# Optimization experiments

Hardware: AMD Instinct MI355X
Metric: run time of the kernel (lower is better)

Reference implementation:

```python
import jax, jax.numpy as jnp
import numpy as np

B, S, IN_DIM, LATENT, SYM = 16, 256, 512, 512, 128
NUM_NODES, NUM_CODES, MAX_OPS, MAX_BUS = 4, 512, 4, 32
HALT_EPS, MAX_SEQ = 1e-3, 256


def setup_inputs() -> dict:
    key = jax.random.key(0)
    ks = jax.random.split(key, 10)

    def lin(k, out_d, in_d, pre=()):
        kw, kb = jax.random.split(k)
        lim = 1.0 / np.sqrt(in_d).astype(np.float32)
        w = jax.random.uniform(kw, pre + (out_d, in_d), minval=-lim, maxval=lim, dtype=jnp.float32)
        b = jax.random.uniform(kb, pre + (out_d,), minval=-lim, maxval=lim, dtype=jnp.float32)
        return w, b

    x = jax.random.normal(ks[0], (B, S, IN_DIM), jnp.float32)
    ipw, ipb = lin(ks[1], LATENT, IN_DIM)
    tp = jax.random.normal(ks[2], (1, MAX_SEQ, LATENT), jnp.float32)
    N = (NUM_NODES,)
    sw, sb = lin(ks[3], SYM, LATENT, N)
    qw, qb = lin(ks[4], 1, SYM, N)
    rw, rb = lin(ks[5], LATENT, 2 * LATENT, N)
    c1w, c1b = lin(ks[6], LATENT, LATENT + SYM, N)
    c2w, c2b = lin(ks[7], LATENT, LATENT, N)
    cb = jax.random.normal(ks[8], (NUM_NODES, NUM_CODES, SYM), jnp.float32)
    return {"x": x, "input_proj_w": ipw, "input_proj_b": ipb, "token_prompts": tp,
            "sym_w": sw, "sym_b": sb, "qry_w": qw, "qry_b": qb,
            "read_w": rw, "read_b": rb, "c1_w": c1w, "c1_b": c1b,
            "c2_w": c2w, "c2_b": c2b, "codebook": cb}


def _forward(x, input_proj_w, input_proj_b, token_prompts, sym_w, sym_b, qry_w, qry_b,
             read_w, read_b, c1_w, c1_b, c2_w, c2_b, codebook):
    Bx, Sx, _ = x.shape
    N = Bx * Sx
    # input projection + positional prompts
    out = jnp.einsum('bsi,li->bsl', x, input_proj_w) + input_proj_b + token_prompts[:, :Sx, :]
    prev_out = out
    active = jnp.ones((Bx, Sx), bool)
    token_tags = jnp.zeros((Bx, Sx, SYM), x.dtype)
    # TensorBus rolling buffers ([max_bus, B, S, dim]); with default cfg the roll branch never fires
    sym_buf = jnp.zeros((MAX_BUS, Bx, Sx, SYM), x.dtype)          # slot 0 = zero tags (initial append)
    out_buf = jnp.zeros((MAX_BUS, Bx, Sx, LATENT), x.dtype).at[0].set(out)
    msg_mask = jnp.zeros((MAX_BUS,), bool).at[0].set(True)
    ptr = 1  # static python int: appends are a fixed unrolled schedule (1 + MAX_OPS*NUM_NODES <= MAX_BUS)
    slot_ids = jnp.arange(MAX_BUS)

    for t in range(MAX_OPS):
        # snapshot of active messages for this op step (get_active)
        snap_active = msg_mask & (slot_ids < ptr)                  # [MAX_BUS]
        syms_flat = sym_buf.reshape(MAX_BUS, N, SYM)
        outs_flat = out_buf.reshape(MAX_BUS, N, LATENT)
        keep_all = jnp.ones((MAX_BUS,), bool)
        for n in range(NUM_NODES):
            # relevance of each bus message per token; inactive slots masked out of argmax
            rel = jnp.einsum('tnd,d->tn', syms_flat, qry_w[n, 0]) + qry_b[n, 0]
            rel = jnp.where(snap_active[:, None], rel, jnp.asarray(-1e9, rel.dtype))
            top = jnp.argmax(rel, axis=0)                          # [N] chosen message per token
            chosen = jnp.take_along_axis(outs_flat, top[None, :, None], axis=0)[0]  # [N, LATENT]
            bus_ctx = chosen.reshape(Bx, Sx, LATENT)
            z = jnp.concatenate([out, bus_ctx], axis=-1)
            z_read = jnp.einsum('bsk,lk->bsl', z, read_w[n]) + read_b[n]
            raw_sym = jnp.einsum('bsl,dl->bsd', z_read, sym_w[n]) + sym_b[n]
            # EMA quantizer (eval): nearest codebook entry by euclidean distance
            flat = raw_sym.reshape(-1, SYM)
            cbn = codebook[n]
            d2 = (jnp.sum(flat * flat, axis=-1, keepdims=True)
                  - 2.0 * flat @ cbn.T + jnp.sum(cbn * cbn, axis=-1))
            idx = jnp.argmin(d2, axis=-1)
            quant = cbn[idx].reshape(Bx, Sx, SYM)
            h = jnp.concatenate([z_read, quant], axis=-1)
            hid = jax.nn.relu(jnp.einsum('bsk,lk->bsl', h, c1_w[n]) + c1_b[n])
            node_out = jnp.einsum('bsl,ol->bso', hid, c2_w[n]) + c2_b[n] + out
            # halting / selective update
            delta = jnp.linalg.norm(node_out - prev_out, axis=-1)
            halt = (delta < HALT_EPS) & active
            assigned = active if t > 0 else jnp.ones_like(active)
            upd = assigned & jnp.logical_not(halt)
            out = jnp.where(upd[..., None], node_out, out)
            token_tags = jnp.where(upd[..., None], quant, token_tags)
            # bus.append
            sym_buf = sym_buf.at[ptr].set(quant)
            out_buf = out_buf.at[ptr].set(node_out)
            msg_mask = msg_mask.at[ptr].set(True)
            ptr += 1
            # keep_mask: messages never selected by any token stay alive
            counts = jnp.zeros((MAX_BUS,), jnp.int32).at[top].add(1)
            keep_all = keep_all & (counts == 0)
            active = active & jnp.logical_not(halt)
            prev_out = out
        # mark_consumed: ones over valid slots ANDed with per-node keep masks at snapshot-active
        # slots (inactive/new slots get True -> faithful to the torch init_global_mask quirk)
        msg_mask = (slot_ids < ptr) & keep_all
    return out


def reference(x, input_proj_w, input_proj_b, token_prompts, sym_w, sym_b, qry_w, qry_b,
              read_w, read_b, c1_w, c1_b, c2_w, c2_b, codebook):
    return _forward(x, input_proj_w, input_proj_b, token_prompts, sym_w, sym_b, qry_w, qry_b,
                    read_w, read_b, c1_w, c1_b, c2_w, c2_b, codebook)
```

## Files before the change

kernel.cpp:

```cpp
#include <hip/hip_runtime.h>
#include <math.h>

namespace {

typedef _Float16 f16;
typedef __attribute__((ext_vector_type(8))) _Float16 f16x8;
typedef __attribute__((ext_vector_type(4))) float f32x4;

constexpr int TOK = 4096;
constexpr int DL  = 512;
constexpr int DS  = 128;
constexpr int NC  = 512;
constexpr int NSLOT = 13;

__device__ __forceinline__ float wsum(float v){
  #pragma unroll
  for(int o=32;o>0;o>>=1) v += __shfl_xor(v,o);
  return v;
}

__device__ __forceinline__ void gload16(const void* g, void* l){
  __builtin_amdgcn_global_load_lds(
      (const __attribute__((address_space(1))) unsigned int*)g,
      (__attribute__((address_space(3))) unsigned int*)l, 16, 0, 0);
}

__device__ __forceinline__ int slotb(int row, int g){
  return (((row ^ ((row>>2)&1))<<2) | (g ^ (row&3))) << 4;
}

template<int AMODE,int EPI>
__global__ __launch_bounds__(256,2) void mgemm(
    const f16* __restrict__ A1h, const f16* __restrict__ A1l,
    const f16* __restrict__ A2h, const f16* __restrict__ A2l,
    const f16* __restrict__ Bh, const f16* __restrict__ Bl,
    const float* __restrict__ bias, const float* __restrict__ res,
    float* __restrict__ Cf, f16* __restrict__ Ch, f16* __restrict__ Cl,
    f16* __restrict__ C2h, f16* __restrict__ C2l,
    float* __restrict__ scpv, int* __restrict__ scpi, int* __restrict__ idxg,
    const float* __restrict__ relc, const int* __restrict__ msg,
    int* __restrict__ cons, int pt, int node,
    int K, int K0)
{
  constexpr int SMB = 16384;
  __shared__ __align__(16) char smem[3*SMB];
  __shared__ int gsel[64];
  __shared__ float redv[4][32];
  __shared__ int   redi[4][32];
  const int tid = threadIdx.x, w = tid>>6, l = tid&63;
  const int m0 = blockIdx.x*64, n0 = blockIdx.y*64;
  const int NK = K>>5, SW = K0>>5;

  if(AMODE==1){
    if(tid<64){
      int m = m0+tid;
      float best = -1e9f; int bs = 0;
      for(int s=0;s<pt;s++){
        float v = msg[s] ? relc[(size_t)((s<<2)+node)*TOK + m] : -1e9f;
        if(v > best){ best=v; bs=s; }
      }
      gsel[tid]=bs;
      cons[bs]=1;
    }
    __syncthreads();
  }
  if(AMODE==2){
    if(tid<64){
      int m = m0+tid;
      float bv = -INFINITY; int bi = 0;
      #pragma unroll
      for(int y=0;y<8;y++){
        float v = scpv[(size_t)y*TOK + m];
        if(v > bv){ bv=v; bi=scpi[(size_t)y*TOK + m]; }
      }
      gsel[tid]=bi;
      idxg[m]=bi;
    }
    __syncthreads();
  }

  const f16* sp[4]; const f16* sp2[4]; int loff[4];
  #pragma unroll
  for(int i=0;i<4;i++){
    int c = 4*w+i;
    int isA = (c<8);
    int plane = isA ? (c>>2) : ((c-8)>>2);
    int cidx  = isA ? (c&3)  : ((c-8)&3);
    loff[i] = (isA?0:8192) + plane*4096 + cidx*1024;
    int s = (cidx<<6) + l;
    int rp = s>>2, row = rp ^ ((rp>>2)&1), g = (s&3) ^ (row&3);
    int g8 = g<<3;
    if(isA){
      int m = m0 + row;
      const f16* p1 = (plane? A1l : A1h) + ((size_t)m<<9) + g8;
      sp[i] = p1;
      if(AMODE==1)      sp2[i] = (plane? A2l : A2h) + ((size_t)gsel[row]<<21) + ((size_t)m<<9) + g8;
      else if(AMODE==2) sp2[i] = (plane? A2l : A2h) + ((size_t)gsel[row]<<7) + g8;
      else              sp2[i] = p1;
    } else {
      sp[i] = (plane? Bl : Bh) + (size_t)(n0+row)*K + g8;
      sp2[i] = sp[i];
    }
  }

  const int wr = w>>1, wc = w&1, q = l>>4, r = l&15;
  int aoff[2], boff[2];
  #pragma unroll
  for(int i=0;i<2;i++) aoff[i] = slotb(32*wr + 16*i + r, q);
  #pragma unroll
  for(int j=0;j<2;j++) boff[j] = 8192 + slotb(32*wc + 16*j + r, q);

  f32x4 acc1[2][2] = {}, acc2[2][2] = {};

  auto advance = [&](int snext){
    #pragma unroll
    for(int i=0;i<4;i++){
      if(AMODE!=0 && (4*w+i)<8 && snext==SW) sp[i] = sp2[i];
      else                                    sp[i] += 32;
    }
  };

  #pragma unroll
  for(int i=0;i<4;i++) gload16(sp[i], smem + loff[i]);
  advance(1);
  #pragma unroll
  for(int i=0;i<4;i++) gload16(sp[i], smem + SMB + loff[i]);
  advance(2);
  asm volatile("s_waitcnt vmcnt(4)" ::: "memory");
  __builtin_amdgcn_s_barrier();

  int roff = 0, soff = 2*SMB;
  for(int kt=0; kt<NK; ++kt){
    const char* Lb = smem + roff;
    f16x8 ah[2], al[2], bh[2], bl[2];
    #pragma unroll
    for(int i=0;i<2;i++){
      ah[i] = *(const f16x8*)(Lb + aoff[i]);
      al[i] = *(const f16x8*)(Lb + 4096 + aoff[i]);
    }
    #pragma unroll
    for(int j=0;j<2;j++){
      bh[j] = *(const f16x8*)(Lb + boff[j]);
      bl[j] = *(const f16x8*)(Lb + 4096 + boff[j]);
    }
    if(kt+2 < NK){
      #pragma unroll
      for(int i=0;i<4;i++) gload16(sp[i], smem + soff + loff[i]);
      advance(kt+3);
    }
    #pragma unroll
    for(int i=0;i<2;i++)
      #pragma unroll
      for(int j=0;j<2;j++){
        acc1[i][j] = __builtin_amdgcn_mfma_f32_16x16x32_f16(ah[i], bh[j], acc1[i][j], 0,0,0);
        acc2[i][j] = __builtin_amdgcn_mfma_f32_16x16x32_f16(ah[i], bl[j], acc2[i][j], 0,0,0);
        acc2[i][j] = __builtin_amdgcn_mfma_f32_16x16x32_f16(al[i], bh[j], acc2[i][j], 0,0,0);
      }
    if(kt+2 < NK){
      asm volatile("s_waitcnt vmcnt(4)" ::: "memory");
      __builtin_amdgcn_s_barrier();
    } else if(kt+1 < NK){
      asm volatile("s_waitcnt vmcnt(0)" ::: "memory");
      __builtin_amdgcn_s_barrier();
    }
    roff = (roff==2*SMB)? 0 : roff+SMB;
    soff = (soff==2*SMB)? 0 : soff+SMB;
  }

  if(EPI!=1){
    #pragma unroll
    for(int i=0;i<2;i++)
      #pragma unroll
      for(int j=0;j<2;j++)
        #pragma unroll
        for(int rr=0;rr<4;rr++){
          int rowm = m0 + 32*wr + 16*i + 4*q + rr;
          int coln = n0 + 32*wc + 16*j + r;
          size_t o = ((size_t)rowm<<9) + coln;
          float v = acc1[i][j][rr] + acc2[i][j][rr]*(1.0f/2048.0f) + bias[coln];
          if(EPI==2) v = fmaxf(v, 0.f);
          if(EPI==3) v += res[o];
          if(EPI==4) v += res[(((size_t)(rowm&255))<<9) + coln];
          if(EPI==3 || EPI==4) Cf[o] = v;
          if(EPI==0 || EPI==2 || EPI==4){
            f16 h = (f16)v;
            Ch[o] = h; Cl[o] = (f16)((v-(float)h)*2048.0f);
          }
          if((EPI==3 || EPI==4) && C2h){
            f16 h = (f16)v;
            C2h[o] = h; C2l[o] = (f16)((v-(float)h)*2048.0f);
          }
        }
  } else {
    #pragma unroll
    for(int i=0;i<2;i++)
      #pragma unroll
      for(int rr=0;rr<4;rr++){
        float v0 = acc1[i][0][rr] + acc2[i][0][rr]*(1.0f/2048.0f) + bias[n0+32*wc+r];
        float v1 = acc1[i][1][rr] + acc2[i][1][rr]*(1.0f/2048.0f) + bias[n0+32*wc+16+r];
        float bv; int bc;
        if(v1 > v0){ bv=v1; bc=n0+32*wc+16+r; } else { bv=v0; bc=n0+32*wc+r; }
        #pragma unroll
        for(int o=1;o<16;o<<=1){
          float ov = __shfl_xor(bv,o); int oi = __shfl_xor(bc,o);
          if(ov>bv || (ov==bv && oi<bc)){ bv=ov; bc=oi; }
        }
        if(r==0){ redv[w][16*i+4*q+rr]=bv; redi[w][16*i+4*q+rr]=bc; }
      }
    __syncthreads();
    if(tid<64){
      int wr2 = tid>>5, li = tid&31;
      float bv = redv[2*wr2][li]; int bc = redi[2*wr2][li];
      float ov = redv[2*wr2+1][li]; int oi = redi[2*wr2+1][li];
      if(ov>bv || (ov==bv && oi<bc)){ bv=ov; bc=oi; }
      scpv[(size_t)blockIdx.y*TOK + m0 + tid] = bv;
      scpi[(size_t)blockIdx.y*TOK + m0 + tid] = bc;
    }
  }
}

__global__ void split_k(const float* __restrict__ src, f16* __restrict__ hi,
                        f16* __restrict__ lo, int n){
  for(int i = blockIdx.x*256 + threadIdx.x; i < n; i += gridDim.x*256){
    float v = src[i];
    f16 h = (f16)v;
    hi[i] = h;
    lo[i] = (f16)((v - (float)h)*2048.0f);
  }
}

struct SplitArg { const float* src; f16* hi; f16* lo; int n; };
struct SplitArgs5 { SplitArg a[5]; };
__global__ void splitm_k(SplitArgs5 A){
  int stride = gridDim.x*256;
  #pragma unroll
  for(int s=0;s<5;s++){
    const float* src = A.a[s].src; f16* hi = A.a[s].hi; f16* lo = A.a[s].lo;
    int n = A.a[s].n;
    for(int i = blockIdx.x*256 + threadIdx.x; i < n; i += stride){
      float v = src[i];
      f16 h = (f16)v;
      hi[i] = h;
      lo[i] = (f16)((v - (float)h)*2048.0f);
    }
  }
}

__global__ __launch_bounds__(256)
void wcomb_k(const float* __restrict__ A, const float* __restrict__ Wall,
             float* __restrict__ C)
{
  constexpr int T=256;
  __shared__ float As[32][68];
  __shared__ float Ws[32][132];
  const int tid = threadIdx.x;
  const int m0 = blockIdx.x*64, n0 = blockIdx.y*128;
  const float* W = Wall + (size_t)(m0>>9)*DS*DL;
  const int ty = tid>>4, tx = tid&15;
  float4 pa[2], pw[4];
  auto loadA = [&](int k0){
    #pragma unroll
    for(int it=0; it<2; ++it){
      int v = tid + T*it; int rr = v>>3, c4 = v&7;
      pa[it] = *(const float4*)(A + (size_t)(m0+rr)*DS + k0 + (c4<<2));
    }
  };
  auto loadW = [&](int k0){
    #pragma unroll
    for(int it=0; it<4; ++it){
      int v = tid + T*it; int rr = v>>5, c4 = v&31;
      pw[it] = *(const float4*)(W + (size_t)(k0+rr)*DL + n0 + (c4<<2));
    }
  };
  float acc[4][8];
  #pragma unroll
  for(int i=0;i<4;i++)
    #pragma unroll
    for(int j=0;j<8;j++) acc[i][j]=0.f;
  loadA(0); loadW(0);
  for(int k0=0; k0<DS; k0+=32){
    __syncthreads();
    #pragma unroll
    for(int it=0; it<2; ++it){
      int v = tid + T*it; int rr=v>>3, c4=v&7;
      As[(c4<<2)+0][rr]=pa[it].x; As[(c4<<2)+1][rr]=pa[it].y;
      As[(c4<<2)+2][rr]=pa[it].z; As[(c4<<2)+3][rr]=pa[it].w;
    }
    #pragma unroll
    for(int it=0; it<4; ++it){
      int v = tid + T*it; int rr=v>>5, c4=v&31;
      *(float4*)&Ws[rr][c4<<2] = pw[it];
    }
    __syncthreads();
    if(k0+32 < DS){ loadA(k0+32); loadW(k0+32); }
    #pragma unroll
    for(int kk=0; kk<32; kk++){
      float4 a4 = *(const float4*)&As[kk][ty<<2];
      float4 b0 = *(const float4*)&Ws[kk][tx<<2];
      float4 b1 = *(const float4*)&Ws[kk][64+(tx<<2)];
      float a[4]={a4.x,a4.y,a4.z,a4.w};
      float b[8]={b0.x,b0.y,b0.z,b0.w,b1.x,b1.y,b1.z,b1.w};
      #pragma unroll
      for(int i=0;i<4;i++)
        #pragma unroll
        for(int j=0;j<8;j++) acc[i][j] = fmaf(a[i], b[j], acc[i][j]);
    }
  }
  #pragma unroll
  for(int i=0;i<4;i++){
    int m = m0 + (ty<<2) + i;
    #pragma unroll
    for(int j=0;j<8;j++){
      int n = n0 + ((j<4)? (tx<<2)+j : 64+(tx<<2)+(j-4));
      C[((size_t)m<<9)+n] = acc[i][j];
    }
  }
}

__global__ void init_k(int* __restrict__ msg, int* __restrict__ act,
                       float* __restrict__ relc, const float* __restrict__ qb,
                       int* __restrict__ cons){
  int i = blockIdx.x*256 + threadIdx.x;
  if(i < TOK){
    act[i] = 1;
    #pragma unroll
    for(int nn=0;nn<4;nn++) relc[nn*TOK + i] = qb[nn];
  }
  if(i < 32){ msg[i] = (i==0) ? 1 : 0; cons[i] = 0; }
}

__global__ void bias2_k(const float* __restrict__ cb, const float* __restrict__ sb,
                        float* __restrict__ b2){
  int row = blockIdx.x*4 + (threadIdx.x>>6);
  int lane = threadIdx.x&63;
  const float* cv = cb + ((size_t)row<<7);
  const float* sbn = sb + ((row>>9)<<7);
  float c0=cv[lane], c1=cv[lane+64];
  float nrm = c0*c0 + c1*c1;
  float dt  = c0*sbn[lane] + c1*sbn[lane+64];
  nrm = wsum(nrm); dt = wsum(dt);
  if(lane==0) b2[row] = dt - 0.5f*nrm;
}

__global__ void mupdate_k(const float* __restrict__ no_, float* __restrict__ out,
                          f16* __restrict__ outh, f16* __restrict__ outl,
                          float* __restrict__ relc, const int* __restrict__ idx,
                          const float* __restrict__ cbn, const float* __restrict__ qw,
                          const float* __restrict__ qb, int* __restrict__ act,
                          int* __restrict__ cons, int* __restrict__ msg,
                          int t, int ptr, int pe){
  int m = blockIdx.x*4 + (threadIdx.x>>6);
  int lane = threadIdx.x&63;
  const float* nrow = no_ + ((size_t)m<<9);
  float* orow = out + ((size_t)m<<9);
  float nv[8]; float s=0.f;
  #pragma unroll
  for(int rr=0;rr<8;rr++){
    int c = lane + (rr<<6);
    nv[rr]=nrow[c];
    float d = nv[rr]-orow[c]; s += d*d;
  }
  s = wsum(s);
  float delta = sqrtf(s);
  int a = act[m];
  int halt = (delta < 1e-3f) && a;
  int assigned = (t>0) ? a : 1;
  int upd = assigned && !halt;
  if(lane==0) act[m] = a && !halt;
  if(upd){
    #pragma unroll
    for(int rr=0;rr<8;rr++){
      int c = lane + (rr<<6);
      float v = nv[rr];
      orow[c] = v;
      f16 h = (f16)v;
      outh[((size_t)m<<9)+c] = h;
      outl[((size_t)m<<9)+c] = (f16)((v-(float)h)*2048.0f);
    }
  }
  if(ptr >= 0){
    const float* qv = cbn + ((size_t)idx[m]<<7);
    float q0=qv[lane], q1=qv[lane+64];
    #pragma unroll
    for(int nn=0;nn<4;nn++){
      float pr = q0*qw[(nn<<7)+lane] + q1*qw[(nn<<7)+64+lane];
      pr = wsum(pr);
      if(lane==0) relc[(size_t)((ptr<<2)+nn)*TOK + m] = pr + qb[nn];
    }
  }
  if(pe >= 0 && blockIdx.x==0 && threadIdx.x < 32){
    int s2 = threadIdx.x;
    msg[s2] = (s2 < pe) && !cons[s2];
    cons[s2] = 0;
  }
}

}

extern "C" void kernel_launch(void* const* d_in, const int* in_sizes, int n_in,
                              void* d_out, int out_size, void* d_ws, size_t ws_size,
                              hipStream_t stream)
{
  (void)in_sizes; (void)n_in; (void)out_size; (void)ws_size;
  const float* x   = (const float*)d_in[0];
  const float* ipw = (const float*)d_in[1];
  const float* ipb = (const float*)d_in[2];
  const float* tp  = (const float*)d_in[3];
  const float* sw  = (const float*)d_in[4];
  const float* sb  = (const float*)d_in[5];
  const float* qw  = (const float*)d_in[6];
  const float* qb  = (const float*)d_in[7];
  const float* rw  = (const float*)d_in[8];
  const float* rb  = (const float*)d_in[9];
  const float* c1w = (const float*)d_in[10];
  const float* c1b = (const float*)d_in[11];
  const float* c2w = (const float*)d_in[12];
  const float* c2b = (const float*)d_in[13];
  const float* cb  = (const float*)d_in[14];
  float* out = (float*)d_out;

  char* p = (char*)d_ws;
  auto alloc = [&](size_t b)->char*{ char* r=p; p += (b+255)&~(size_t)255; return r; };
  f16* slabh = (f16*)alloc((size_t)NSLOT*TOK*DL*2);
  f16* slabl = (f16*)alloc((size_t)NSLOT*TOK*DL*2);
  f16* outh  = (f16*)alloc((size_t)TOK*DL*2);
  f16* outl  = (f16*)alloc((size_t)TOK*DL*2);
  f16* zh    = (f16*)alloc((size_t)TOK*DL*2);
  f16* zl    = (f16*)alloc((size_t)TOK*DL*2);
  f16* hh    = (f16*)alloc((size_t)TOK*DL*2);
  f16* hl    = (f16*)alloc((size_t)TOK*DL*2);
  float* sn  = (float*)alloc((size_t)TOK*DL*4);
  f16* rwh   = (f16*)alloc((size_t)4*DL*1024*2);
  f16* rwl   = (f16*)alloc((size_t)4*DL*1024*2);
  f16* c1h   = (f16*)alloc((size_t)4*DL*640*2);
  f16* c1l   = (f16*)alloc((size_t)4*DL*640*2);
  f16* c2h   = (f16*)alloc((size_t)4*DL*DL*2);
  f16* c2l   = (f16*)alloc((size_t)4*DL*DL*2);
  f16* wch   = (f16*)alloc((size_t)4*NC*DL*2);
  f16* wcl   = (f16*)alloc((size_t)4*NC*DL*2);
  f16* iph   = (f16*)alloc((size_t)DL*DL*2);
  f16* ipl   = (f16*)alloc((size_t)DL*DL*2);
  f16* cbh   = (f16*)alloc((size_t)4*NC*DS*2);
  f16* cbl   = (f16*)alloc((size_t)4*NC*DS*2);
  float* b2  = (float*)alloc(4*NC*4);
  float* relc= (float*)alloc((size_t)NSLOT*4*TOK*4);
  float* scpv= (float*)alloc((size_t)8*TOK*4);
  int* scpi  = (int*)alloc((size_t)8*TOK*4);
  int* idxb  = (int*)alloc(TOK*4);
  int* act   = (int*)alloc(TOK*4);
  int* msg   = (int*)alloc(256);
  int* cons  = (int*)alloc(256);

  dim3 G(64,8), B(256);

  init_k<<<16,256,0,stream>>>(msg, act, relc, qb, cons);
  bias2_k<<<512,256,0,stream>>>(cb, sb, b2);
  wcomb_k<<<dim3(32,4),B,0,stream>>>(cb, sw, sn);
  split_k<<<2048,256,0,stream>>>(x, hh, hl, TOK*DL);
  SplitArgs5 sa;
  sa.a[0] = { ipw, iph, ipl, DL*DL };
  sa.a[1] = { rw,  rwh, rwl, 4*DL*1024 };
  sa.a[2] = { c1w, c1h, c1l, 4*DL*640 };
  sa.a[3] = { c2w, c2h, c2l, 4*DL*DL };
  sa.a[4] = { cb,  cbh, cbl, 4*NC*DS };
  splitm_k<<<2048,256,0,stream>>>(sa);
  split_k<<<1024,256,0,stream>>>(sn, wch, wcl, 4*NC*DL);

  mgemm<0,4><<<G,B,0,stream>>>(hh,hl, nullptr,nullptr, iph,ipl,
      ipb, tp, out, outh,outl, slabh,slabl,
      nullptr,nullptr,nullptr, nullptr,nullptr,nullptr, 0,0, DL, DL);

  int ptr = 1;
  for(int t=0;t<4;t++){
    int pt = 1 + 4*t;
    for(int n=0;n<4;n++){
      mgemm<1,0><<<G,B,0,stream>>>(outh,outl, slabh,slabl,
          rwh+(size_t)n*DL*1024, rwl+(size_t)n*DL*1024, rb+(size_t)n*DL,
          nullptr, nullptr, zh,zl, nullptr,nullptr,
          nullptr,nullptr,nullptr, relc, msg, cons, pt, n, 1024, 512);
      mgemm<0,1><<<G,B,0,stream>>>(zh,zl, nullptr,nullptr,
          wch+(size_t)n*NC*DL, wcl+(size_t)n*NC*DL, b2+(size_t)n*NC,
          nullptr, nullptr, nullptr,nullptr, nullptr,nullptr,
          scpv,scpi,nullptr, nullptr,nullptr,nullptr, 0,0, 512, 512);
      mgemm<2,2><<<G,B,0,stream>>>(zh,zl, cbh+(size_t)n*NC*DS, cbl+(size_t)n*NC*DS,
          c1h+(size_t)n*DL*640, c1l+(size_t)n*DL*640, c1b+(size_t)n*DL,
          nullptr, nullptr, hh,hl, nullptr,nullptr,
          scpv,scpi,idxb, nullptr,nullptr,nullptr, 0,0, 640, 512);
      f16* sph = (t<3) ? slabh + ((size_t)ptr<<21) : nullptr;
      f16* spl = (t<3) ? slabl + ((size_t)ptr<<21) : nullptr;
      mgemm<0,3><<<G,B,0,stream>>>(hh,hl, nullptr,nullptr,
          c2h+(size_t)n*DL*DL, c2l+(size_t)n*DL*DL, c2b+(size_t)n*DL,
          out, sn, nullptr,nullptr, sph,spl,
          nullptr,nullptr,nullptr, nullptr,nullptr,nullptr, 0,0, 512, 512);
      mupdate_k<<<1024,256,0,stream>>>(sn, out, outh,outl, relc, idxb,
          cb+(size_t)n*NC*DS, qw, qb, act, cons, msg, t,
          (t<3)? ptr : -1, (n==3 && t<3)? (1+4*(t+1)) : -1);
      ptr++;
    }
  }
}
```

Baseline: 1.290 ms.

## Deepen GEMM pipeline to four LDS stages with register double-buffered fragments

The MFMA GEMM main loop moves from a 3-buffer LDS ring to a 4-buffer ring with three tiles prefetched. The loop is unrolled by two, and LDS fragments for the next k-tile are loaded into a second register set while the current tile's MFMAs run. The goal is to hide LDS read latency and global-load latency behind compute. In exchange, LDS use rises to 64KB plus extras, which may limit the two-blocks-per-CU occupancy, and register pressure increases. The loop assumes NK is even.

```diff
diff --git a/kernel.cpp b/kernel.cpp
--- a/kernel.cpp
+++ b/kernel.cpp
@@ -43,7 +43,7 @@
     int K, int K0)
 {
   constexpr int SMB = 16384;
-  __shared__ __align__(16) char smem[3*SMB];
+  __shared__ __align__(16) char smem[4*SMB];
   __shared__ int gsel[64];
   __shared__ float redv[4][32];
   __shared__ int   redi[4][32];
@@ -119,52 +119,54 @@
       else                                    sp[i] += 32;
     }
   };
-
-  #pragma unroll
-  for(int i=0;i<4;i++) gload16(sp[i], smem + loff[i]);
-  advance(1);
-  #pragma unroll
-  for(int i=0;i<4;i++) gload16(sp[i], smem + SMB + loff[i]);
-  advance(2);
-  asm volatile("s_waitcnt vmcnt(4)" ::: "memory");
-  __builtin_amdgcn_s_barrier();
-
-  int roff = 0, soff = 2*SMB;
-  for(int kt=0; kt<NK; ++kt){
-    const char* Lb = smem + roff;
-    f16x8 ah[2], al[2], bh[2], bl[2];
-    #pragma unroll
-    for(int i=0;i<2;i++){
-      ah[i] = *(const f16x8*)(Lb + aoff[i]);
-      al[i] = *(const f16x8*)(Lb + 4096 + aoff[i]);
-    }
-    #pragma unroll
-    for(int j=0;j<2;j++){
-      bh[j] = *(const f16x8*)(Lb + boff[j]);
-      bl[j] = *(const f16x8*)(Lb + 4096 + boff[j]);
-    }
-    if(kt+2 < NK){
-      #pragma unroll
-      for(int i=0;i<4;i++) gload16(sp[i], smem + soff + loff[i]);
-      advance(kt+3);
-    }
+  auto stage = [&](int buf){
+    char* dst = smem + buf*SMB;
+    #pragma unroll
+    for(int i=0;i<4;i++) gload16(sp[i], dst + loff[i]);
+  };
+
+  f16x8 X[8], Y[8];
+  auto ldfrag = [&](const char* Lb, f16x8* F){
+    F[0] = *(const f16x8*)(Lb + aoff[0]);
+    F[1] = *(const f16x8*)(Lb + aoff[1]);
+    F[2] = *(const f16x8*)(Lb + 4096 + aoff[0]);
+    F[3] = *(const f16x8*)(Lb + 4096 + aoff[1]);
+    F[4] = *(const f16x8*)(Lb + boff[0]);
+    F[5] = *(const f16x8*)(Lb + boff[1]);
+    F[6] = *(const f16x8*)(Lb + 4096 + boff[0]);
+    F[7] = *(const f16x8*)(Lb + 4096 + boff[1]);
+  };
+  auto domfma = [&](const f16x8* F){
     #pragma unroll
     for(int i=0;i<2;i++)
       #pragma unroll
       for(int j=0;j<2;j++){
-        acc1[i][j] = __builtin_amdgcn_mfma_f32_16x16x32_f16(ah[i], bh[j], acc1[i][j], 0,0,0);
-        acc2[i][j] = __builtin_amdgcn_mfma_f32_16x16x32_f16(ah[i], bl[j], acc2[i][j], 0,0,0);
-        acc2[i][j] = __builtin_amdgcn_mfma_f32_16x16x32_f16(al[i], bh[j], acc2[i][j], 0,0,0);
+        acc1[i][j] = __builtin_amdgcn_mfma_f32_16x16x32_f16(F[i],   F[4+j], acc1[i][j], 0,0,0);
+        acc2[i][j] = __builtin_amdgcn_mfma_f32_16x16x32_f16(F[i],   F[6+j], acc2[i][j], 0,0,0);
+        acc2[i][j] = __builtin_amdgcn_mfma_f32_16x16x32_f16(F[2+i], F[4+j], acc2[i][j], 0,0,0);
       }
-    if(kt+2 < NK){
-      asm volatile("s_waitcnt vmcnt(4)" ::: "memory");
-      __builtin_amdgcn_s_barrier();
-    } else if(kt+1 < NK){
-      asm volatile("s_waitcnt vmcnt(0)" ::: "memory");
-      __builtin_amdgcn_s_barrier();
-    }
-    roff = (roff==2*SMB)? 0 : roff+SMB;
-    soff = (soff==2*SMB)? 0 : soff+SMB;
+  };
+
+  stage(0); advance(1);
+  stage(1); advance(2);
+  stage(2); advance(3);
+  asm volatile("s_waitcnt vmcnt(4)" ::: "memory");
+  __builtin_amdgcn_s_barrier();
+  ldfrag(smem, X);
+
+  for(int kt=0; kt<NK; kt+=2){
+    ldfrag(smem + ((kt+1)&3)*SMB, Y);
+    if(kt+3 < NK){ stage((kt+3)&3); advance(kt+4); }
+    domfma(X);
+    if(kt+3 < NK)      { asm volatile("s_waitcnt vmcnt(4)" ::: "memory"); }
+    else if(kt+2 < NK) { asm volatile("s_waitcnt vmcnt(0)" ::: "memory"); }
+    __builtin_amdgcn_s_barrier();
+    if(kt+2 < NK) ldfrag(smem + ((kt+2)&3)*SMB, X);
+    if(kt+4 < NK){ stage((kt+4)&3); advance(kt+5); }
+    domfma(Y);
+    if(kt+4 < NK)      { asm volatile("s_waitcnt vmcnt(4)" ::: "memory"); }
+    else if(kt+3 < NK) { asm volatile("s_waitcnt vmcnt(0)" ::: "memory"); }
+    if(kt+2 < NK) __builtin_amdgcn_s_barrier();
   }
 
   if(EPI!=1){
```

New measurement: 1.318 ms. 2.2% more time.

## Run each 64x64 GEMM tile on a single wave instead of four

Applied to the files above, without the earlier changes.

The split-precision GEMM now uses 64-thread blocks: one wavefront loads the whole 64x64 A and B tiles into the triple-buffered LDS and computes all 16 MFMA sub-tiles itself. This removes the block-wide barriers and the cross-wave LDS reduction in the argmax epilogue. In exchange each wave issues four times as many global-to-LDS loads and holds 4x4 accumulator pairs in registers. The grid stays at 512 blocks, so only about 512 waves are in flight per GEMM, which lowers occupancy and latency hiding.

```diff
diff --git a/kernel.cpp b/kernel.cpp
--- a/kernel.cpp
+++ b/kernel.cpp
@@ -30,7 +30,7 @@
 }
 
 template<int AMODE,int EPI>
-__global__ __launch_bounds__(256,2) void mgemm(
+__global__ __launch_bounds__(64,2) void mgemm(
     const f16* __restrict__ A1h, const f16* __restrict__ A1l,
     const f16* __restrict__ A2h, const f16* __restrict__ A2l,
     const f16* __restrict__ Bh, const f16* __restrict__ Bl,
@@ -45,137 +45,139 @@
   constexpr int SMB = 16384;
   __shared__ __align__(16) char smem[3*SMB];
   __shared__ int gsel[64];
-  __shared__ float redv[4][32];
-  __shared__ int   redi[4][32];
-  const int tid = threadIdx.x, w = tid>>6, l = tid&63;
+  const int l = threadIdx.x;
   const int m0 = blockIdx.x*64, n0 = blockIdx.y*64;
   const int NK = K>>5, SW = K0>>5;
 
   if(AMODE==1){
-    if(tid<64){
-      int m = m0+tid;
+    {
+      int m = m0+l;
       float best = -1e9f; int bs = 0;
       for(int s=0;s<pt;s++){
         float v = msg[s] ? relc[(size_t)((s<<2)+node)*TOK + m] : -1e9f;
         if(v > best){ best=v; bs=s; }
       }
-      gsel[tid]=bs;
+      gsel[l]=bs;
       cons[bs]=1;
     }
     __syncthreads();
   }
   if(AMODE==2){
-    if(tid<64){
-      int m = m0+tid;
+    {
+      int m = m0+l;
       float bv = -INFINITY; int bi = 0;
       #pragma unroll
       for(int y=0;y<8;y++){
         float v = scpv[(size_t)y*TOK + m];
         if(v > bv){ bv=v; bi=scpi[(size_t)y*TOK + m]; }
       }
-      gsel[tid]=bi;
+      gsel[l]=bi;
       idxg[m]=bi;
     }
     __syncthreads();
   }
 
-  const f16* sp[4]; const f16* sp2[4]; int loff[4];
+  const int rl = (l>>2) ^ ((l>>4)&1);
+  const int g8 = ((l&3) ^ (rl&3))<<3;
+
+  const f16* cA[8]; const f16* cB[8]; const f16* p2[8];
+  #pragma unroll
+  for(int c=0;c<4;c++){
+    cA[c]   = A1h + ((size_t)(m0+16*c+rl)<<9) + g8;
+    cA[4+c] = A1l + ((size_t)(m0+16*c+rl)<<9) + g8;
+    cB[c]   = Bh + (size_t)(n0+16*c+rl)*K + g8;
+    cB[4+c] = Bl + (size_t)(n0+16*c+rl)*K + g8;
+  }
+  if(AMODE==1){
+    #pragma unroll
+    for(int c=0;c<4;c++){
+      size_t off = ((size_t)gsel[16*c+rl]<<21) + ((size_t)(m0+16*c+rl)<<9) + g8;
+      p2[c] = A2h + off; p2[4+c] = A2l + off;
+    }
+  }
+  if(AMODE==2){
+    #pragma unroll
+    for(int c=0;c<4;c++){
+      size_t off = ((size_t)gsel[16*c+rl]<<7) + g8;
+      p2[c] = A2h + off; p2[4+c] = A2l + off;
+    }
+  }
+
+  const int q = l>>4, r = l&15;
+  int aoff[4], boff[4];
   #pragma unroll
   for(int i=0;i<4;i++){
-    int c = 4*w+i;
-    int isA = (c<8);
-    int plane = isA ? (c>>2) : ((c-8)>>2);
-    int cidx  = isA ? (c&3)  : ((c-8)&3);
-    loff[i] = (isA?0:8192) + plane*4096 + cidx*1024;
-    int s = (cidx<<6) + l;
-    int rp = s>>2, row = rp ^ ((rp>>2)&1), g = (s&3) ^ (row&3);
-    int g8 = g<<3;
-    if(isA){
-      int m = m0 + row;
-      const f16* p1 = (plane? A1l : A1h) + ((size_t)m<<9) + g8;
-      sp[i] = p1;
-      if(AMODE==1)      sp2[i] = (plane? A2l : A2h) + ((size_t)gsel[row]<<21) + ((size_t)m<<9) + g8;
-      else if(AMODE==2) sp2[i] = (plane? A2l : A2h) + ((size_t)gsel[row]<<7) + g8;
-      else              sp2[i] = p1;
-    } else {
-      sp[i] = (plane? Bl : Bh) + (size_t)(n0+row)*K + g8;
-      sp2[i] = sp[i];
-    }
-  }
-
-  const int wr = w>>1, wc = w&1, q = l>>4, r = l&15;
-  int aoff[2], boff[2];
-  #pragma unroll
-  for(int i=0;i<2;i++) aoff[i] = slotb(32*wr + 16*i + r, q);
-  #pragma unroll
-  for(int j=0;j<2;j++) boff[j] = 8192 + slotb(32*wc + 16*j + r, q);
-
-  f32x4 acc1[2][2] = {}, acc2[2][2] = {};
+    aoff[i] = slotb(16*i + r, q);
+    boff[i] = 8192 + slotb(16*i + r, q);
+  }
+
+  f32x4 acc1[4][4] = {}, acc2[4][4] = {};
 
   auto advance = [&](int snext){
     #pragma unroll
-    for(int i=0;i<4;i++){
-      if(AMODE!=0 && (4*w+i)<8 && snext==SW) sp[i] = sp2[i];
-      else                                    sp[i] += 32;
-    }
+    for(int c=0;c<8;c++){
+      if(AMODE!=0 && snext==SW) cA[c] = p2[c];
+      else                      cA[c] += 32;
+    }
+    #pragma unroll
+    for(int c=0;c<8;c++) cB[c] += 32;
   };
-
-  #pragma unroll
-  for(int i=0;i<4;i++) gload16(sp[i], smem + loff[i]);
-  advance(1);
-  #pragma unroll
-  for(int i=0;i<4;i++) gload16(sp[i], smem + SMB + loff[i]);
-  advance(2);
-  asm volatile("s_waitcnt vmcnt(4)" ::: "memory");
-  __builtin_amdgcn_s_barrier();
-
-  int roff = 0, soff = 2*SMB;
+  auto stage = [&](int buf){
+    char* dst = smem + buf*SMB;
+    #pragma unroll
+    for(int c=0;c<8;c++){
+      int lo = (c<4) ? c*1024 : 4096 + (c-4)*1024;
+      gload16(cA[c], dst + lo);
+    }
+    #pragma unroll
+    for(int c=0;c<8;c++){
+      int lo = 8192 + ((c<4) ? c*1024 : 4096 + (c-4)*1024);
+      gload16(cB[c], dst + lo);
+    }
+  };
+
+  stage(0); advance(1);
+  stage(1); advance(2);
+  asm volatile("s_waitcnt vmcnt(16)" ::: "memory");
+
+  int rb = 0;
   for(int kt=0; kt<NK; ++kt){
-    const char* Lb = smem + roff;
-    f16x8 ah[2], al[2], bh[2], bl[2];
-    #pragma unroll
-    for(int i=0;i<2;i++){
-      ah[i] = *(const f16x8*)(Lb + aoff[i]);
-      al[i] = *(const f16x8*)(Lb + 4096 + aoff[i]);
-    }
-    #pragma unroll
-    for(int j=0;j<2;j++){
+    const char* Lb = smem + rb*SMB;
+    f16x8 bh[4], bl[4];
+    #pragma unroll
+    for(int j=0;j<4;j++){
       bh[j] = *(const f16x8*)(Lb + boff[j]);
       bl[j] = *(const f16x8*)(Lb + 4096 + boff[j]);
     }
     if(kt+2 < NK){
+      int sb = rb+2; if(sb>=3) sb-=3;
+      stage(sb); advance(kt+3);
+    }
+    #pragma unroll
+    for(int i=0;i<4;i++){
+      f16x8 ah = *(const f16x8*)(Lb + aoff[i]);
+      f16x8 al = *(const f16x8*)(Lb + 4096 + aoff[i]);
       #pragma unroll
-      for(int i=0;i<4;i++) gload16(sp[i], smem + soff + loff[i]);
-      advance(kt+3);
-    }
-    #pragma unroll
-    for(int i=0;i<2;i++)
+      for(int j=0;j<4;j++){
+        acc1[i][j] = __builtin_amdgcn_mfma_f32_16x16x32_f16(ah, bh[j], acc1[i][j], 0,0,0);
+        acc2[i][j] = __builtin_amdgcn_mfma_f32_16x16x32_f16(ah, bl[j], acc2[i][j], 0,0,0);
+        acc2[i][j] = __builtin_amdgcn_mfma_f32_16x16x32_f16(al, bh[j], acc2[i][j], 0,0,0);
+      }
+    }
+    if(kt+2 < NK){ asm volatile("s_waitcnt vmcnt(16)" ::: "memory"); }
+    else if(kt+1 < NK){ asm volatile("s_waitcnt vmcnt(0)" ::: "memory"); }
+    rb = (rb==2)? 0 : rb+1;
+  }
+
+  if(EPI!=1){
+    #pragma unroll
+    for(int i=0;i<4;i++)
       #pragma unroll
-      for(int j=0;j<2;j++){
-        acc1[i][j] = __builtin_amdgcn_mfma_f32_16x16x32_f16(ah[i], bh[j], acc1[i][j], 0,0,0);
-        acc2[i][j] = __builtin_amdgcn_mfma_f32_16x16x32_f16(ah[i], bl[j], acc2[i][j], 0,0,0);
-        acc2[i][j] = __builtin_amdgcn_mfma_f32_16x16x32_f16(al[i], bh[j], acc2[i][j], 0,0,0);
-      }
-    if(kt+2 < NK){
-      asm volatile("s_waitcnt vmcnt(4)" ::: "memory");
-      __builtin_amdgcn_s_barrier();
-    } else if(kt+1 < NK){
-      asm volatile("s_waitcnt vmcnt(0)" ::: "memory");
-      __builtin_amdgcn_s_barrier();
-    }
-    roff = (roff==2*SMB)? 0 : roff+SMB;
-    soff = (soff==2*SMB)? 0 : soff+SMB;
-  }
-
-  if(EPI!=1){
-    #pragma unroll
-    for(int i=0;i<2;i++)
-      #pragma unroll
-      for(int j=0;j<2;j++)
+      for(int j=0;j<4;j++)
         #pragma unroll
         for(int rr=0;rr<4;rr++){
-          int rowm = m0 + 32*wr + 16*i + 4*q + rr;
-          int coln = n0 + 32*wc + 16*j + r;
+          int rowm = m0 + 16*i + 4*q + rr;
+          int coln = n0 + 16*j + r;
           size_t o = ((size_t)rowm<<9) + coln;
           float v = acc1[i][j][rr] + acc2[i][j][rr]*(1.0f/2048.0f) + bias[coln];
           if(EPI==2) v = fmaxf(v, 0.f);
@@ -193,29 +195,27 @@
         }
   } else {
     #pragma unroll
-    for(int i=0;i<2;i++)
+    for(int i=0;i<4;i++)
       #pragma unroll
       for(int rr=0;rr<4;rr++){
-        float v0 = acc1[i][0][rr] + acc2[i][0][rr]*(1.0f/2048.0f) + bias[n0+32*wc+r];
-        float v1 = acc1[i][1][rr] + acc2[i][1][rr]*(1.0f/2048.0f) + bias[n0+32*wc+16+r];
-        float bv; int bc;
-        if(v1 > v0){ bv=v1; bc=n0+32*wc+16+r; } else { bv=v0; bc=n0+32*wc+r; }
+        float bv = -INFINITY; int bc = 0;
+        #pragma unroll
+        for(int j=0;j<4;j++){
+          float v = acc1[i][j][rr] + acc2[i][j][rr]*(1.0f/2048.0f) + bias[n0+16*j+r];
+          int c = n0 + 16*j + r;
+          if(v > bv){ bv=v; bc=c; }
+        }
         #pragma unroll
         for(int o=1;o<16;o<<=1){
           float ov = __shfl_xor(bv,o); int oi = __shfl_xor(bc,o);
           if(ov>bv || (ov==bv && oi<bc)){ bv=ov; bc=oi; }
         }
-        if(r==0){ redv[w][16*i+4*q+rr]=bv; redi[w][16*i+4*q+rr]=bc; }
+        if(r==0){
+          int rowm = m0 + 16*i + 4*q + rr;
+          scpv[(size_t)blockIdx.y*TOK + rowm] = bv;
+          scpi[(size_t)blockIdx.y*TOK + rowm] = bc;
+        }
       }
-    __syncthreads();
-    if(tid<64){
-      int wr2 = tid>>5, li = tid&31;
-      float bv = redv[2*wr2][li]; int bc = redi[2*wr2][li];
-      float ov = redv[2*wr2+1][li]; int oi = redi[2*wr2+1][li];
-      if(ov>bv || (ov==bv && oi<bc)){ bv=ov; bc=oi; }
-      scpv[(size_t)blockIdx.y*TOK + m0 + tid] = bv;
-      scpi[(size_t)blockIdx.y*TOK + m0 + tid] = bc;
-    }
   }
 }
 
@@ -451,7 +451,7 @@
   int* msg   = (int*)alloc(256);
   int* cons  = (int*)alloc(256);
 
-  dim3 G(64,8), B(256);
+  dim3 G(64,8), B(256), Bm(64);
 
   init_k<<<16,256,0,stream>>>(msg, act, relc, qb, cons);
   bias2_k<<<512,256,0,stream>>>(cb, sb, b2);
@@ -466,7 +466,7 @@
   splitm_k<<<2048,256,0,stream>>>(sa);
   split_k<<<1024,256,0,stream>>>(sn, wch, wcl, 4*NC*DL);
 
-  mgemm<0,4><<<G,B,0,stream>>>(hh,hl, nullptr,nullptr, iph,ipl,
+  mgemm<0,4><<<G,Bm,0,stream>>>(hh,hl, nullptr,nullptr, iph,ipl,
       ipb, tp, out, outh,outl, slabh,slabl,
       nullptr,nullptr,nullptr, nullptr,nullptr,nullptr, 0,0, DL, DL);
 
@@ -474,21 +474,21 @@
   for(int t=0;t<4;t++){
     int pt = 1 + 4*t;
     for(int n=0;n<4;n++){
-      mgemm<1,0><<<G,B,0,stream>>>(outh,outl, slabh,slabl,
+      mgemm<1,0><<<G,Bm,0,stream>>>(outh,outl, slabh,slabl,
           rwh+(size_t)n*DL*1024, rwl+(size_t)n*DL*1024, rb+(size_t)n*DL,
           nullptr, nullptr, zh,zl, nullptr,nullptr,
           nullptr,nullptr,nullptr, relc, msg, cons, pt, n, 1024, 512);
-      mgemm<0,1><<<G,B,0,stream>>>(zh,zl, nullptr,nullptr,
+      mgemm<0,1><<<G,Bm,0,stream>>>(zh,zl, nullptr,nullptr,
           wch+(size_t)n*NC*DL, wcl+(size_t)n*NC*DL, b2+(size_t)n*NC,
           nullptr, nullptr, nullptr,nullptr, nullptr,nullptr,
           scpv,scpi,nullptr, nullptr,nullptr,nullptr, 0,0, 512, 512);
-      mgemm<2,2><<<G,B,0,stream>>>(zh,zl, cbh+(size_t)n*NC*DS, cbl+(size_t)n*NC*DS,
+      mgemm<2,2><<<G,Bm,0,stream>>>(zh,zl, cbh+(size_t)n*NC*DS, cbl+(size_t)n*NC*DS,
           c1h+(size_t)n*DL*640, c1l+(size_t)n*DL*640, c1b+(size_t)n*DL,
           nullptr, nullptr, hh,hl, nullptr,nullptr,
           scpv,scpi,idxb, nullptr,nullptr,nullptr, 0,0, 640, 512);
       f16* sph = (t<3) ? slabh + ((size_t)ptr<<21) : nullptr;
       f16* spl = (t<3) ? slabl + ((size_t)ptr<<21) : nullptr;
-      mgemm<0,3><<<G,B,0,stream>>>(hh,hl, nullptr,nullptr,
+      mgemm<0,3><<<G,Bm,0,stream>>>(hh,hl, nullptr,nullptr,
           c2h+(size_t)n*DL*DL, c2l+(size_t)n*DL*DL, c2b+(size_t)n*DL,
           out, sn, nullptr,nullptr, sph,spl,
           nullptr,nullptr,nullptr, nullptr,nullptr,nullptr, 0,0, 512, 512);
```

After: 1.997 ms. 54.8% more time.

## Precompute codebook-times-c1 weight products and gather them in the c1 epilogue

Applied to the files above, without the earlier changes.

The c1 layer's input is the concatenation of z and the selected codebook entry. The codebook part of that GEMM is now precomputed once per node as codebook @ c1_w[:,512:]^T in fp32. In the c1 GEMM the K loop shrinks from 640 to 512, using a new leading-dimension parameter. The epilogue adds the gathered precomputed row for each token's code index before the ReLU. This removes per-token GEMM work and the A-operand switch, at the cost of an extra setup kernel, a 4MB buffer and scattered epilogue reads.

```diff
diff --git a/kernel.cpp b/kernel.cpp
--- a/kernel.cpp
+++ b/kernel.cpp
@@ -40,7 +40,8 @@
     float* __restrict__ scpv, int* __restrict__ scpi, int* __restrict__ idxg,
     const float* __restrict__ relc, const int* __restrict__ msg,
     int* __restrict__ cons, int pt, int node,
-    int K, int K0)
+    const float* __restrict__ pq,
+    int K, int K0, int ldb)
 {
   constexpr int SMB = 16384;
   __shared__ __align__(16) char smem[3*SMB];
@@ -64,7 +65,7 @@
     }
     __syncthreads();
   }
-  if(AMODE==2){
+  if(AMODE==3){
     if(tid<64){
       int m = m0+tid;
       float bv = -INFINITY; int bi = 0;
@@ -94,11 +95,10 @@
       int m = m0 + row;
       const f16* p1 = (plane? A1l : A1h) + ((size_t)m<<9) + g8;
       sp[i] = p1;
-      if(AMODE==1)      sp2[i] = (plane? A2l : A2h) + ((size_t)gsel[row]<<21) + ((size_t)m<<9) + g8;
-      else if(AMODE==2) sp2[i] = (plane? A2l : A2h) + ((size_t)gsel[row]<<7) + g8;
-      else              sp2[i] = p1;
+      if(AMODE==1) sp2[i] = (plane? A2l : A2h) + ((size_t)gsel[row]<<21) + ((size_t)m<<9) + g8;
+      else         sp2[i] = p1;
     } else {
-      sp[i] = (plane? Bl : Bh) + (size_t)(n0+row)*K + g8;
+      sp[i] = (plane? Bl : Bh) + (size_t)(n0+row)*ldb + g8;
       sp2[i] = sp[i];
     }
   }
@@ -115,7 +115,7 @@
   auto advance = [&](int snext){
     #pragma unroll
     for(int i=0;i<4;i++){
-      if(AMODE!=0 && (4*w+i)<8 && snext==SW) sp[i] = sp2[i];
+      if(AMODE==1 && (4*w+i)<8 && snext==SW) sp[i] = sp2[i];
       else                                    sp[i] += 32;
     }
   };
@@ -174,15 +174,16 @@
       for(int j=0;j<2;j++)
         #pragma unroll
         for(int rr=0;rr<4;rr++){
-          int rowm = m0 + 32*wr + 16*i + 4*q + rr;
+          int lrow = 32*wr + 16*i + 4*q + rr;
+          int rowm = m0 + lrow;
           int coln = n0 + 32*wc + 16*j + r;
           size_t o = ((size_t)rowm<<9) + coln;
           float v = acc1[i][j][rr] + acc2[i][j][rr]*(1.0f/2048.0f) + bias[coln];
-          if(EPI==2) v = fmaxf(v, 0.f);
+          if(EPI==5){ v += pq[((size_t)gsel[lrow]<<9) + coln]; v = fmaxf(v, 0.f); }
           if(EPI==3) v += res[o];
           if(EPI==4) v += res[(((size_t)(rowm&255))<<9) + coln];
           if(EPI==3 || EPI==4) Cf[o] = v;
-          if(EPI==0 || EPI==2 || EPI==4){
+          if(EPI==0 || EPI==4 || EPI==5){
             f16 h = (f16)v;
             Ch[o] = h; Cl[o] = (f16)((v-(float)h)*2048.0f);
           }
@@ -290,6 +291,81 @@
     for(int it=0; it<4; ++it){
       int v = tid + T*it; int rr=v>>5, c4=v&31;
       *(float4*)&Ws[rr][c4<<2] = pw[it];
+    }
+    __syncthreads();
+    if(k0+32 < DS){ loadA(k0+32); loadW(k0+32); }
+    #pragma unroll
+    for(int kk=0; kk<32; kk++){
+      float4 a4 = *(const float4*)&As[kk][ty<<2];
+      float4 b0 = *(const float4*)&Ws[kk][tx<<2];
+      float4 b1 = *(const float4*)&Ws[kk][64+(tx<<2)];
+      float a[4]={a4.x,a4.y,a4.z,a4.w};
+      float b[8]={b0.x,b0.y,b0.z,b0.w,b1.x,b1.y,b1.z,b1.w};
+      #pragma unroll
+      for(int i=0;i<4;i++)
+        #pragma unroll
+        for(int j=0;j<8;j++) acc[i][j] = fmaf(a[i], b[j], acc[i][j]);
+    }
+  }
+  #pragma unroll
+  for(int i=0;i<4;i++){
+    int m = m0 + (ty<<2) + i;
+    #pragma unroll
+    for(int j=0;j<8;j++){
+      int n = n0 + ((j<4)? (tx<<2)+j : 64+(tx<<2)+(j-4));
+      C[((size_t)m<<9)+n] = acc[i][j];
+    }
+  }
+}
+
+__global__ __launch_bounds__(256)
+void prequant_k(const float* __restrict__ cbp, const float* __restrict__ c1wp,
+                float* __restrict__ pq)
+{
+  constexpr int T=256;
+  __shared__ float As[32][68];
+  __shared__ float Ws[32][132];
+  const int tid = threadIdx.x;
+  const int nz = blockIdx.z;
+  const int m0 = blockIdx.x*64, n0 = blockIdx.y*128;
+  const float* A = cbp  + (size_t)nz*NC*DS;
+  const float* W = c1wp + (size_t)nz*DL*640 + 512;
+  float* C = pq + (size_t)nz*NC*DL;
+  const int ty = tid>>4, tx = tid&15;
+  float4 pa[2], pw[4];
+  auto loadA = [&](int k0){
+    #pragma unroll
+    for(int it=0; it<2; ++it){
+      int v = tid + T*it; int rr = v>>3, c4 = v&7;
+      pa[it] = *(const float4*)(A + (size_t)(m0+rr)*DS + k0 + (c4<<2));
+    }
+  };
+  auto loadW = [&](int k0){
+    #pragma unroll
+    for(int it=0; it<4; ++it){
+      int v = tid + T*it; int rr = v>>3, c4 = v&7;
+      pw[it] = *(const float4*)(W + (size_t)(n0+rr)*640 + k0 + (c4<<2));
+    }
+  };
+  float acc[4][8];
+  #pragma unroll
+  for(int i=0;i<4;i++)
+    #pragma unroll
+    for(int j=0;j<8;j++) acc[i][j]=0.f;
+  loadA(0); loadW(0);
+  for(int k0=0; k0<DS; k0+=32){
+    __syncthreads();
+    #pragma unroll
+    for(int it=0; it<2; ++it){
+      int v = tid + T*it; int rr=v>>3, c4=v&7;
+      As[(c4<<2)+0][rr]=pa[it].x; As[(c4<<2)+1][rr]=pa[it].y;
+      As[(c4<<2)+2][rr]=pa[it].z; As[(c4<<2)+3][rr]=pa[it].w;
+    }
+    #pragma unroll
+    for(int it=0; it<4; ++it){
+      int v = tid + T*it; int rr=v>>3, c4=v&7;
+      Ws[(c4<<2)+0][rr]=pw[it].x; Ws[(c4<<2)+1][rr]=pw[it].y;
+      Ws[(c4<<2)+2][rr]=pw[it].z; Ws[(c4<<2)+3][rr]=pw[it].w;
     }
     __syncthreads();
     if(k0+32 < DS){ loadA(k0+32); loadW(k0+32); }
@@ -442,6 +518,7 @@
   f16* ipl   = (f16*)alloc((size_t)DL*DL*2);
   f16* cbh   = (f16*)alloc((size_t)4*NC*DS*2);
   f16* cbl   = (f16*)alloc((size_t)4*NC*DS*2);
+  float* pq  = (float*)alloc((size_t)4*NC*DL*4);
   float* b2  = (float*)alloc(4*NC*4);
   float* relc= (float*)alloc((size_t)NSLOT*4*TOK*4);
   float* scpv= (float*)alloc((size_t)8*TOK*4);
@@ -456,6 +533,7 @@
   init_k<<<16,256,0,stream>>>(msg, act, relc, qb, cons);
   bias2_k<<<512,256,0,stream>>>(cb, sb, b2);
   wcomb_k<<<dim3(32,4),B,0,stream>>>(cb, sw, sn);
+  prequant_k<<<dim3(8,4,4),B,0,stream>>>(cb, c1w, pq);
   split_k<<<2048,256,0,stream>>>(x, hh, hl, TOK*DL);
   SplitArgs5 sa;
   sa.a[0] = { ipw, iph, ipl, DL*DL };
@@ -468,7 +546,8 @@
 
   mgemm<0,4><<<G,B,0,stream>>>(hh,hl, nullptr,nullptr, iph,ipl,
       ipb, tp, out, outh,outl, slabh,slabl,
-      nullptr,nullptr,nullptr, nullptr,nullptr,nullptr, 0,0, DL, DL);
+      nullptr,nullptr,nullptr, nullptr,nullptr,nullptr, 0,0,
+      nullptr, DL, DL, DL);
 
   int ptr = 1;
   for(int t=0;t<4;t++){
@@ -477,21 +556,25 @@
       mgemm<1,0><<<G,B,0,stream>>>(outh,outl, slabh,slabl,
           rwh+(size_t)n*DL*1024, rwl+(size_t)n*DL*1024, rb+(size_t)n*DL,
           nullptr, nullptr, zh,zl, nullptr,nullptr,
-          nullptr,nullptr,nullptr, relc, msg, cons, pt, n, 1024, 512);
+          nullptr,nullptr,nullptr, relc, msg, cons, pt, n,
+          nullptr, 1024, 512, 1024);
       mgemm<0,1><<<G,B,0,stream>>>(zh,zl, nullptr,nullptr,
           wch+(size_t)n*NC*DL, wcl+(size_t)n*NC*DL, b2+(size_t)n*NC,
           nullptr, nullptr, nullptr,nullptr, nullptr,nullptr,
-          scpv,scpi,nullptr, nullptr,nullptr,nullptr, 0,0, 512, 512);
-      mgemm<2,2><<<G,B,0,stream>>>(zh,zl, cbh+(size_t)n*NC*DS, cbl+(size_t)n*NC*DS,
+          scpv,scpi,nullptr, nullptr,nullptr,nullptr, 0,0,
+          nullptr, 512, 512, 512);
+      mgemm<3,5><<<G,B,0,stream>>>(zh,zl, nullptr,nullptr,
           c1h+(size_t)n*DL*640, c1l+(size_t)n*DL*640, c1b+(size_t)n*DL,
           nullptr, nullptr, hh,hl, nullptr,nullptr,
-          scpv,scpi,idxb, nullptr,nullptr,nullptr, 0,0, 640, 512);
+          scpv,scpi,idxb, nullptr,nullptr,nullptr, 0,0,
+          pq+(size_t)n*NC*DL, 512, 512, 640);
       f16* sph = (t<3) ? slabh + ((size_t)ptr<<21) : nullptr;
       f16* spl = (t<3) ? slabl + ((size_t)ptr<<21) : nullptr;
       mgemm<0,3><<<G,B,0,stream>>>(hh,hl, nullptr,nullptr,
           c2h+(size_t)n*DL*DL, c2l+(size_t)n*DL*DL, c2b+(size_t)n*DL,
           out, sn, nullptr,nullptr, sph,spl,
-          nullptr,nullptr,nullptr, nullptr,nullptr,nullptr, 0,0, 512, 512);
+          nullptr,nullptr,nullptr, nullptr,nullptr,nullptr, 0,0,
+          nullptr, 512, 512, 512);
       mupdate_k<<<1024,256,0,stream>>>(sn, out, outh,outl, relc, idxb,
           cb+(size_t)n*NC*DS, qw, qb, act, cons, msg, t,
           (t<3)? ptr : -1, (n==3 && t<3)? (1+4*(t+1)) : -1);
```

After: 1.280 ms, median of 2. Within noise of the previous version (-0.8%).
